# Optimization experiments

Measured on AMD Instinct MI355X. Metric: run time of the kernel, lower is better.

## Reference

```python
import jax, jax.numpy as jnp
import numpy as np

N, B, E, H, G, L = 128, 2, 512, 1024, 50, 3
RBF_RADIUS = 12.0
AVG_LEN = 60.0


def _resmlp(h, Win, bin_, Wh, bh, Wout, bout):
    # input proj + activation, residual hidden blocks, linear head
    h = jax.nn.gelu(h @ Win + bin_, approximate=False)
    for i in range(Wh.shape[0]):  # fixed small number of layers
        h = h + jax.nn.gelu(h @ Wh[i] + bh[i], approximate=False)
    return h @ Wout + bout


def setup_inputs() -> dict:
    key = jax.random.key(0)
    ks = jax.random.split(key, 20)
    s_in = 1.0 / np.sqrt(3 * E)
    s_h = 1.0 / np.sqrt(H)
    s_g = 1.0 / np.sqrt(G)
    return {
        'x': jax.random.normal(ks[0], (N, B, E), jnp.float32),
        'dist': jax.random.uniform(ks[1], (N, N, B), jnp.float32),
        'vec_hat': jax.random.normal(ks[2], (N, N, B, 3), jnp.float32),
        'mask': jnp.ones((B, N), dtype=bool),
        'rbf_W': jax.random.normal(ks[3], (G, E), jnp.float32) * s_g,
        'rbf_b': jnp.zeros((E,), jnp.float32),
        'e_Win': jax.random.normal(ks[4], (3 * E, H), jnp.float32) * s_in,
        'e_bin': jnp.zeros((H,), jnp.float32),
        'e_Wh': jax.random.normal(ks[5], (L, H, H), jnp.float32) * s_h,
        'e_bh': jnp.zeros((L, H), jnp.float32),
        'e_Wout': jax.random.normal(ks[6], (H, 1), jnp.float32) * s_h,
        'e_bout': jnp.zeros((1,), jnp.float32),
        'f_Win': jax.random.normal(ks[7], (3 * E, H), jnp.float32) * s_in,
        'f_bin': jnp.zeros((H,), jnp.float32),
        'f_Wh': jax.random.normal(ks[8], (L, H, H), jnp.float32) * s_h,
        'f_bh': jnp.zeros((L, H), jnp.float32),
        'f_Wout': jax.random.normal(ks[9], (H, 1), jnp.float32) * s_h,
        'f_bout': jnp.zeros((1,), jnp.float32),
    }


def reference(x, dist, vec_hat, mask, rbf_W, rbf_b, e_Win, e_bin, e_Wh, e_bh,
              e_Wout, e_bout, f_Win, f_bin, f_Wh, f_bh, f_Wout, f_bout):
    # Gaussian RBF expansion + linear projection to embed_dim
    offset = jnp.linspace(0.0, RBF_RADIUS, G)
    coeff = -0.5 / (offset[1] - offset[0]) ** 2
    g = jnp.exp(coeff * (dist[..., None] - offset) ** 2)       # (N,N,B,G)
    rbf = g @ rbf_W + rbf_b                                    # (N,N,B,E)

    # all-pairs concat feature: [x_i, x_j, rbf_ij]  -> (N,N,B,3E)
    feat = jnp.concatenate([
        jnp.broadcast_to(x[:, None], rbf.shape),
        jnp.broadcast_to(x[None, :], rbf.shape),
        rbf,
    ], axis=-1)

    entries = (mask.T[:, None] & mask.T[None, :])[..., None].astype(feat.dtype)  # (N,N,B,1)

    energy_pairs = _resmlp(feat, e_Win, e_bin, e_Wh, e_bh, e_Wout, e_bout)       # (N,N,B,1)
    force_pairs = _resmlp(feat, f_Win, f_bin, f_Wh, f_bh, f_Wout, f_bout) * vec_hat  # (N,N,B,3)

    energy = (energy_pairs * entries).sum((0, 1)) / AVG_LEN ** 2  # (B,1)
    forces = (force_pairs * entries).sum(0) / AVG_LEN             # (N,B,3)
    # torch: forces.transpose(0,1)[mask]; mask is all-True here, so this is a reshape
    forces = jnp.swapaxes(forces, 0, 1).reshape(-1, 3)            # (B*N,3)
    return energy, forces
```

## Files before the change

kernel.cpp:

```cpp
#include <hip/hip_runtime.h>
#include <stdint.h>

typedef __bf16 bf16x8 __attribute__((ext_vector_type(8)));
typedef __bf16 bf16x4 __attribute__((ext_vector_type(4)));
typedef float  f32x4  __attribute__((ext_vector_type(4)));
typedef unsigned int u32;

__device__ __forceinline__ void gl_lds16(const void* gptr, void* lptr) {
    __builtin_amdgcn_global_load_lds(
        (const __attribute__((address_space(1))) u32*)gptr,
        (__attribute__((address_space(3))) u32*)lptr,
        16, 0, 0);
}

__device__ __forceinline__ float gelu_f(float x) {
    float u = 0.7978845608f * x * (1.0f + 0.044715f * x * x);
    float e = __expf(2.0f * u);
    float t = 1.0f - 2.0f / (e + 1.0f);
    return 0.5f * x * (1.0f + t);
}

#define MEMFENCE __asm__ __volatile__("" ::: "memory")

__global__ void zero_out(float* __restrict__ o, int n) {
    int i = blockIdx.x * 256 + threadIdx.x;
    if (i < n) o[i] = 0.0f;
}

__global__ __launch_bounds__(256)
void transpose_multi(const float* __restrict__ src0, const float* __restrict__ src1,
                     __bf16* __restrict__ dst0, __bf16* __restrict__ dst1,
                     int K, int Ncols, int perBranch) {
    const int z = blockIdx.z;
    const int branch = z / perBranch;
    const int l = z - branch * perBranch;
    const size_t elems = (size_t)K * Ncols;
    const float* src = (branch ? src1 : src0) + (size_t)l * elems;
    __bf16* dst = (branch ? dst1 : dst0) + (size_t)l * elems;

    __shared__ float tile[64][65];
    const int bk = blockIdx.x * 64;
    const int bn = blockIdx.y * 64;
    const int tid = threadIdx.x;
    const int tr = tid >> 4;
    const int tc = (tid & 15) * 4;
#pragma unroll
    for (int p = 0; p < 4; ++p) {
        const int r = tr + p * 16;
        float4 v = *(const float4*)&src[(size_t)(bk + r) * Ncols + bn + tc];
        tile[r][tc] = v.x; tile[r][tc + 1] = v.y;
        tile[r][tc + 2] = v.z; tile[r][tc + 3] = v.w;
    }
    __syncthreads();
#pragma unroll
    for (int p = 0; p < 4; ++p) {
        const int rn = tr + p * 16;
        bf16x4 o;
        o[0] = (__bf16)tile[tc + 0][rn];
        o[1] = (__bf16)tile[tc + 1][rn];
        o[2] = (__bf16)tile[tc + 2][rn];
        o[3] = (__bf16)tile[tc + 3][rn];
        *(bf16x4*)&dst[(size_t)(bn + rn) * K + bk + tc] = o;
    }
}

__global__ void f32_to_bf16(const float* __restrict__ s, __bf16* __restrict__ d, int n) {
    int idx = blockIdx.x * 256 + threadIdx.x;
    if (idx * 4 < n) {
        float4 v = *(const float4*)(s + idx * 4);
        bf16x4 o;
        o[0] = (__bf16)v.x; o[1] = (__bf16)v.y; o[2] = (__bf16)v.z; o[3] = (__bf16)v.w;
        *(bf16x4*)(d + idx * 4) = o;
    }
}

__global__ void build_M1(const float* __restrict__ rbfW, const float* __restrict__ rbf_b,
                         __bf16* __restrict__ M1) {
    int t = blockIdx.x * 256 + threadIdx.x;
    int r = t >> 8;
    int c = (t & 255) * 2;
    float v0 = 0.f, v1 = 0.f;
    if (r < 50)       { v0 = rbfW[r * 512 + c]; v1 = rbfW[r * 512 + c + 1]; }
    else if (r == 50) { v0 = rbf_b[c];          v1 = rbf_b[c + 1]; }
    M1[r * 512 + c] = (__bf16)v0;
    M1[r * 512 + c + 1] = (__bf16)v1;
}

__global__ __launch_bounds__(256)
void build_G(const float* __restrict__ dist, __bf16* __restrict__ G) {
    const int t = threadIdx.x;
    const int row = blockIdx.x * 32 + (t >> 3);
    const int c0 = (t & 7) * 8;
    const float sp = 12.0f / 49.0f;
    const float coeff = -0.5f / (sp * sp);
    const float d = dist[row];
    bf16x8 v;
#pragma unroll
    for (int q = 0; q < 8; ++q) {
        const int k = c0 + q;
        float val;
        if (k < 50)       { float tt = d - (float)k * sp; val = __expf(coeff * tt * tt); }
        else if (k == 50) val = 1.0f;
        else              val = 0.0f;
        v[q] = (__bf16)val;
    }
    *(bf16x8*)(G + (size_t)row * 64 + c0) = v;
}

template <int NK, int NBN, int MODE, bool DUAL, int MINW, bool SWZ>
__global__ __launch_bounds__(256, MINW)
void gemm_k(const __bf16* __restrict__ A0, const __bf16* __restrict__ A1,
            const __bf16* __restrict__ B0, const __bf16* __restrict__ B1,
            int lda, int ldb, int ldc,
            const float* __restrict__ bias0, const float* __restrict__ bias1,
            __bf16* __restrict__ C0, __bf16* __restrict__ C1,
            float* __restrict__ Cf0, float* __restrict__ Cf1,
            const float* __restrict__ P0, const float* __restrict__ P1,
            const float* __restrict__ wout0, const float* __restrict__ wout1,
            float* __restrict__ dot0, float* __restrict__ dot1) {
    constexpr int NBS = (NBN == 16) ? 4 : (NBN == 8) ? 3 : 0;
    __shared__ __align__(16) __bf16 As[3][128 * 32];
    __shared__ __align__(16) __bf16 Bs[3][128 * 32];

    const int tid = threadIdx.x;
    int bn, bm, branch = 0;
    if constexpr (SWZ) {
        const int x = blockIdx.x & 7;
        const int slot = blockIdx.x >> 3;
        bn = slot & (NBN - 1);
        int grp = x + ((slot >> NBS) << 3);
        if constexpr (DUAL) {
            const int half = (gridDim.x >> NBS) >> 1;
            branch = (grp >= half);
            if (branch) grp -= half;
        }
        bm = grp;
    } else {
        int f2 = blockIdx.x;
        if constexpr (DUAL) {
            const int half = gridDim.x >> 1;
            branch = (f2 >= half);
            if (branch) f2 -= half;
        }
        bn = f2 & (NBN - 1);
        bm = f2 >> NBS;
    }
    const int w = tid >> 6;
    const int lane = tid & 63;

    const __bf16* Ab = (DUAL && branch) ? A1 : A0;
    const __bf16* Bb = (DUAL && branch) ? B1 : B0;

    const int r0 = tid >> 2;
    const int s0 = tid & 3;
    const char* gA0 = (const char*)Ab + (size_t)(bm * 128 + r0) * lda + s0 * 16;
    const char* gA1 = gA0 + (size_t)64 * lda;
    const char* gB0 = (const char*)Bb + (size_t)(bn * 128 + r0) * ldb + s0 * 16;
    const char* gB1 = gB0 + (size_t)64 * ldb;

    char* lA0 = (char*)&As[0][0] + w * 1024;
    char* lA1 = (char*)&As[1][0] + w * 1024;
    char* lA2 = (char*)&As[2][0] + w * 1024;
    char* lB0 = (char*)&Bs[0][0] + w * 1024;
    char* lB1 = (char*)&Bs[1][0] + w * 1024;
    char* lB2 = (char*)&Bs[2][0] + w * 1024;

    const int wm = (w >> 1) & 1;
    const int wn = w & 1;
    const int lm = lane & 15;
    const int ko = (lane >> 4) << 3;
    const int fo = (wm * 64 + lm) * 32 + ko;
    const int go = (wn * 64 + lm) * 32 + ko;
    const __bf16* pA0 = &As[0][0] + fo;
    const __bf16* pA1 = &As[1][0] + fo;
    const __bf16* pA2 = &As[2][0] + fo;
    const __bf16* pB0 = &Bs[0][0] + go;
    const __bf16* pB1 = &Bs[1][0] + go;
    const __bf16* pB2 = &Bs[2][0] + go;

    f32x4 acc[4][4];
    const f32x4 zero = {0.0f, 0.0f, 0.0f, 0.0f};
#pragma unroll
    for (int i = 0; i < 4; ++i)
#pragma unroll
        for (int j = 0; j < 4; ++j) acc[i][j] = zero;

    auto stage = [&](int buf) {
        char* la = (buf == 0) ? lA0 : (buf == 1) ? lA1 : lA2;
        char* lb = (buf == 0) ? lB0 : (buf == 1) ? lB1 : lB2;
        gl_lds16(gA0, la); gl_lds16(gA1, la + 4096);
        gl_lds16(gB0, lb); gl_lds16(gB1, lb + 4096);
        gA0 += 64; gA1 += 64; gB0 += 64; gB1 += 64;
    };
    auto compute = [&](int buf) {
        const __bf16* pa = (buf == 0) ? pA0 : (buf == 1) ? pA1 : pA2;
        const __bf16* pb = (buf == 0) ? pB0 : (buf == 1) ? pB1 : pB2;
        bf16x8 af[4], bfg[4];
#pragma unroll
        for (int i = 0; i < 4; ++i) {
            af[i]  = *(const bf16x8*)(pa + i * 512);
            bfg[i] = *(const bf16x8*)(pb + i * 512);
        }
#pragma unroll
        for (int mi = 0; mi < 4; ++mi)
#pragma unroll
            for (int ni = 0; ni < 4; ++ni)
                acc[mi][ni] = __builtin_amdgcn_mfma_f32_16x16x32_bf16(
                    af[mi], bfg[ni], acc[mi][ni], 0, 0, 0);
    };
    auto iterstep = [&](int cbuf, int sbuf) {
        MEMFENCE;
        __builtin_amdgcn_s_waitcnt(0xF74);
        __builtin_amdgcn_s_barrier();
        MEMFENCE;
        compute(cbuf);
        MEMFENCE;
        stage(sbuf);
        MEMFENCE;
    };

    stage(0);
    stage(1);
    constexpr int NIT = NK - 2;
    constexpr int NG = NIT / 3;
    constexpr int NR = NIT % 3;
    for (int g = 0; g < NG; ++g) {
        iterstep(0, 2);
        iterstep(1, 0);
        iterstep(2, 1);
    }
    if constexpr (NR >= 1) iterstep(0, 2);
    if constexpr (NR >= 2) iterstep(1, 0);
    MEMFENCE;
    __builtin_amdgcn_s_waitcnt(0xF74);
    __builtin_amdgcn_s_barrier();
    MEMFENCE;
    compute((NK - 2) % 3);
    MEMFENCE;
    __builtin_amdgcn_s_waitcnt(0xF70);
    __builtin_amdgcn_s_barrier();
    MEMFENCE;
    compute((NK - 1) % 3);

    const int col0 = bn * 128 + wn * 64 + lm;
    const int row0 = bm * 128 + wm * 64 + ((lane >> 4) << 2);
    const int ldaE = lda >> 1;

    float rowdot[16];
    if constexpr (MODE == 1) {
#pragma unroll
        for (int q = 0; q < 16; ++q) rowdot[q] = 0.0f;
    }

    const bool side = (MODE == 2) && (bn >= 8);
    const float* bp = (MODE == 2) ? (side ? bias1 : bias0)
                                  : ((DUAL && branch) ? bias1 : bias0);
    __bf16* Cout = (MODE == 2) ? (side ? C1 : C0)
                               : ((DUAL && branch) ? C1 : C0);
    const float* woutb = (MODE == 1) ? ((DUAL && branch) ? wout1 : wout0) : nullptr;

#pragma unroll
    for (int ni = 0; ni < 4; ++ni) {
        const int gn = col0 + ni * 16;
        const int gnl = (MODE == 2) ? (gn & 1023) : gn;
        float bv = 0.0f;
        if constexpr (MODE <= 2) bv = bp[gnl];
        float wv = 0.0f;
        if constexpr (MODE == 1) wv = woutb[gn];

        float res[16];
        if constexpr (MODE == 0 || MODE == 1) {
#pragma unroll
            for (int mi = 0; mi < 4; ++mi)
#pragma unroll
                for (int rr = 0; rr < 4; ++rr)
                    res[mi * 4 + rr] =
                        (float)Ab[(size_t)(row0 + mi * 16 + rr) * ldaE + gn];
        } else if constexpr (MODE == 2) {
#pragma unroll
            for (int mi = 0; mi < 4; ++mi)
#pragma unroll
                for (int rr = 0; rr < 4; ++rr) {
                    const int gm = row0 + mi * 16 + rr;
                    const int p0row = ((gm >> 8) << 1) | (gm & 1);
                    const int p1row = gm & 255;
                    res[mi * 4 + rr] = P0[(size_t)p0row * 2048 + gn]
                                     + P1[(size_t)p1row * 2048 + gn];
                }
        }
        MEMFENCE;

#pragma unroll
        for (int mi = 0; mi < 4; ++mi) {
#pragma unroll
            for (int rr = 0; rr < 4; ++rr) {
                const int gm = row0 + mi * 16 + rr;
                const float a = acc[mi][ni][rr];
                if constexpr (MODE == 0) {
                    float v = gelu_f(a + bv) + res[mi * 4 + rr];
                    Cout[(size_t)gm * ldc + gn] = (__bf16)v;
                } else if constexpr (MODE == 1) {
                    float v = gelu_f(a + bv) + res[mi * 4 + rr];
                    rowdot[mi * 4 + rr] += v * wv;
                } else if constexpr (MODE == 2) {
                    float v = a + bv + res[mi * 4 + rr];
                    Cout[(size_t)gm * ldc + gnl] = (__bf16)gelu_f(v);
                } else if constexpr (MODE == 3) {
                    float* Cfw = (DUAL && branch) ? Cf1 : Cf0;
                    Cfw[(size_t)gm * ldc + gn] = a;
                } else {
                    C0[(size_t)gm * ldc + gn] = (__bf16)a;
                }
            }
        }
    }

    if constexpr (MODE == 1) {
#pragma unroll
        for (int s = 1; s < 16; s <<= 1)
#pragma unroll
            for (int q = 0; q < 16; ++q) rowdot[q] += __shfl_xor(rowdot[q], s);
        if (lm == 0) {
            float* dotb = (DUAL && branch) ? dot1 : dot0;
            float* dp = dotb + (size_t)(bn * 2 + wn) * 32768 + row0;
#pragma unroll
            for (int q = 0; q < 16; ++q)
                dp[(q >> 2) * 16 + (q & 3)] = rowdot[q];
        }
    }
}

template <int MODE, bool DUAL>
__global__ __launch_bounds__(512, 2)
void gemm256(const __bf16* __restrict__ A0, const __bf16* __restrict__ A1,
             const __bf16* __restrict__ B0, const __bf16* __restrict__ B1,
             const float* __restrict__ bias0, const float* __restrict__ bias1,
             __bf16* __restrict__ C0, __bf16* __restrict__ C1,
             const float* __restrict__ wout0, const float* __restrict__ wout1,
             float* __restrict__ dot0, float* __restrict__ dot1) {
    __shared__ __align__(16) char ldsbuf[131072];

    const int tid = threadIdx.x;
    const int nxg = gridDim.x >> 3;
    const int id = (blockIdx.x & 7) * nxg + (blockIdx.x >> 3);
    const int bn = id & 3;
    int rest = id >> 2;
    int branch = 0;
    if constexpr (DUAL) { branch = rest >> 7; rest &= 127; }
    const int bm = rest;

    const __bf16* __restrict__ Ab = (DUAL && branch) ? A1 : A0;
    const __bf16* __restrict__ Bb = (DUAL && branch) ? B1 : B0;

    const int w = tid >> 6;
    const int lane = tid & 63;

    const int srow = tid >> 3;
    const int scol = ((tid & 7) * 16) ^ (((tid >> 3) & 7) << 4);
    const char* gA = (const char*)Ab + (size_t)(bm * 256 + srow) * 2048 + scol;
    const char* gB = (const char*)Bb + (size_t)(bn * 256 + srow) * 2048 + scol;
    char* stBase = ldsbuf + w * 1024;

    auto stageTile = [&](int kt, int buf) {
        const size_t ko = (size_t)kt * 128;
        char* d = stBase + buf * 65536;
        gl_lds16(gA + ko,              d);
        gl_lds16(gA + ko +  64 * 2048, d + 8192);
        gl_lds16(gA + ko + 128 * 2048, d + 16384);
        gl_lds16(gA + ko + 192 * 2048, d + 24576);
        gl_lds16(gB + ko,              d + 32768);
        gl_lds16(gB + ko +  64 * 2048, d + 40960);
        gl_lds16(gB + ko + 128 * 2048, d + 49152);
        gl_lds16(gB + ko + 192 * 2048, d + 57344);
    };

    const int wm = w >> 2, wn = w & 3;
    const int lm = lane & 15, lq = lane >> 4;
    const int xorm = (lm & 7) << 4;
    const int rA0 = (wm * 128 + lm) * 128;
    const int rB0 = 32768 + (wn * 64 + lm) * 128;
    const int offk0 = (lq * 16) ^ xorm;
    const int offk1 = (64 + lq * 16) ^ xorm;

    f32x4 acc[8][4];
    const f32x4 zero = {0.0f, 0.0f, 0.0f, 0.0f};
#pragma unroll
    for (int i = 0; i < 8; ++i)
#pragma unroll
        for (int j = 0; j < 4; ++j) acc[i][j] = zero;

    auto body = [&](int kt, bool last) {
        const char* Lb = ldsbuf + (kt & 1) * 65536;
        MEMFENCE;
        if (last) __builtin_amdgcn_s_waitcnt(0xF70);
        else      __builtin_amdgcn_s_waitcnt(0xF78);
        __builtin_amdgcn_s_barrier();
        MEMFENCE;
        bf16x8 a0[8], b0[4], a1[8], b1[4];
#pragma unroll
        for (int mi = 0; mi < 8; ++mi)
            a0[mi] = *(const bf16x8*)(Lb + rA0 + mi * 2048 + offk0);
#pragma unroll
        for (int ni = 0; ni < 4; ++ni)
            b0[ni] = *(const bf16x8*)(Lb + rB0 + ni * 2048 + offk0);
        __builtin_amdgcn_s_setprio(1);
#pragma unroll
        for (int mi = 0; mi < 4; ++mi)
#pragma unroll
            for (int ni = 0; ni < 4; ++ni)
                acc[mi][ni] = __builtin_amdgcn_mfma_f32_16x16x32_bf16(
                    a0[mi], b0[ni], acc[mi][ni], 0, 0, 0);
        __builtin_amdgcn_s_setprio(0);
#pragma unroll
        for (int mi = 0; mi < 8; ++mi)
            a1[mi] = *(const bf16x8*)(Lb + rA0 + mi * 2048 + offk1);
#pragma unroll
        for (int ni = 0; ni < 4; ++ni)
            b1[ni] = *(const bf16x8*)(Lb + rB0 + ni * 2048 + offk1);
        __builtin_amdgcn_s_setprio(1);
#pragma unroll
        for (int mi = 4; mi < 8; ++mi)
#pragma unroll
            for (int ni = 0; ni < 4; ++ni)
                acc[mi][ni] = __builtin_amdgcn_mfma_f32_16x16x32_bf16(
                    a0[mi], b0[ni], acc[mi][ni], 0, 0, 0);
        __builtin_amdgcn_s_setprio(0);
        MEMFENCE;
        __builtin_amdgcn_s_waitcnt(0xC07F);
        __builtin_amdgcn_s_barrier();
        MEMFENCE;
        if (!last && kt < 14) stageTile(kt + 2, kt & 1);
        MEMFENCE;
        __builtin_amdgcn_s_setprio(1);
#pragma unroll
        for (int mi = 0; mi < 4; ++mi)
#pragma unroll
            for (int ni = 0; ni < 4; ++ni)
                acc[mi][ni] = __builtin_amdgcn_mfma_f32_16x16x32_bf16(
                    a1[mi], b1[ni], acc[mi][ni], 0, 0, 0);
#pragma unroll
        for (int mi = 4; mi < 8; ++mi)
#pragma unroll
            for (int ni = 0; ni < 4; ++ni)
                acc[mi][ni] = __builtin_amdgcn_mfma_f32_16x16x32_bf16(
                    a1[mi], b1[ni], acc[mi][ni], 0, 0, 0);
        __builtin_amdgcn_s_setprio(0);
    };

    stageTile(0, 0);
    stageTile(1, 1);
    for (int kt = 0; kt < 15; ++kt) body(kt, false);
    body(15, true);

    const int row0 = bm * 256 + wm * 128 + lq * 4;
    const int col0 = bn * 256 + wn * 64 + lm;
    const float* __restrict__ bp = (DUAL && branch) ? bias1 : bias0;
    float bv[4];
#pragma unroll
    for (int ni = 0; ni < 4; ++ni) bv[ni] = bp[col0 + ni * 16];

    if constexpr (MODE == 0) {
        __bf16* __restrict__ Cw = (DUAL && branch) ? C1 : C0;
#pragma unroll
        for (int mi = 0; mi < 8; ++mi) {
            float res[16];
#pragma unroll
            for (int ni = 0; ni < 4; ++ni)
#pragma unroll
                for (int rr = 0; rr < 4; ++rr)
                    res[ni * 4 + rr] =
                        (float)Ab[(size_t)(row0 + mi * 16 + rr) * 1024 + col0 + ni * 16];
            MEMFENCE;
#pragma unroll
            for (int ni = 0; ni < 4; ++ni)
#pragma unroll
                for (int rr = 0; rr < 4; ++rr) {
                    float v = gelu_f(acc[mi][ni][rr] + bv[ni]) + res[ni * 4 + rr];
                    Cw[(size_t)(row0 + mi * 16 + rr) * 1024 + col0 + ni * 16] = (__bf16)v;
                }
        }
    } else {
        const float* __restrict__ wb = (DUAL && branch) ? wout1 : wout0;
        float wv[4];
#pragma unroll
        for (int ni = 0; ni < 4; ++ni) wv[ni] = wb[col0 + ni * 16];
        float rowdot[32];
#pragma unroll
        for (int q = 0; q < 32; ++q) rowdot[q] = 0.0f;
#pragma unroll
        for (int mi = 0; mi < 8; ++mi) {
            float res[16];
#pragma unroll
            for (int ni = 0; ni < 4; ++ni)
#pragma unroll
                for (int rr = 0; rr < 4; ++rr)
                    res[ni * 4 + rr] =
                        (float)Ab[(size_t)(row0 + mi * 16 + rr) * 1024 + col0 + ni * 16];
            MEMFENCE;
#pragma unroll
            for (int ni = 0; ni < 4; ++ni)
#pragma unroll
                for (int rr = 0; rr < 4; ++rr) {
                    float v = gelu_f(acc[mi][ni][rr] + bv[ni]) + res[ni * 4 + rr];
                    rowdot[mi * 4 + rr] += v * wv[ni];
                }
        }
#pragma unroll
        for (int s = 1; s < 16; s <<= 1)
#pragma unroll
            for (int q = 0; q < 32; ++q) rowdot[q] += __shfl_xor(rowdot[q], s);
        if (lm == 0) {
            float* __restrict__ db = (DUAL && branch) ? dot1 : dot0;
            float* dp = db + (size_t)(bn * 4 + wn) * 32768 + bm * 256 + wm * 128;
#pragma unroll
            for (int mi = 0; mi < 8; ++mi)
#pragma unroll
                for (int rr = 0; rr < 4; ++rr)
                    dp[mi * 16 + lq * 4 + rr] = rowdot[mi * 4 + rr];
        }
    }
}

__global__ __launch_bounds__(128)
void finalize(const float* __restrict__ dot_e, const float* __restrict__ dot_f,
              const float* __restrict__ eb, const float* __restrict__ fb,
              const float* __restrict__ vec, float* __restrict__ out) {
    const int bj = blockIdx.x;
    const int bb = bj >> 7, jj = bj & 127;
    const int i = threadIdx.x;
    const int m = (i * 128 + jj) * 2 + bb;
    float e = eb[0], f = fb[0];
#pragma unroll
    for (int s = 0; s < 16; ++s) {
        e += dot_e[(size_t)s * 32768 + m];
        f += dot_f[(size_t)s * 32768 + m];
    }
    f *= (1.0f / 60.0f);
    float fx = f * vec[(size_t)m * 3 + 0];
    float fy = f * vec[(size_t)m * 3 + 1];
    float fz = f * vec[(size_t)m * 3 + 2];
#pragma unroll
    for (int off = 32; off > 0; off >>= 1) {
        e  += __shfl_down(e, off);
        fx += __shfl_down(fx, off);
        fy += __shfl_down(fy, off);
        fz += __shfl_down(fz, off);
    }
    __shared__ float red[2][4];
    const int wv = i >> 6, lane = i & 63;
    if (lane == 0) { red[wv][0] = e; red[wv][1] = fx; red[wv][2] = fy; red[wv][3] = fz; }
    __syncthreads();
    if (i == 0) {
        atomicAdd(&out[bb], (red[0][0] + red[1][0]) * (1.0f / 3600.0f));
        float* fo = out + 2 + bj * 3;
        fo[0] = red[0][1] + red[1][1];
        fo[1] = red[0][2] + red[1][2];
        fo[2] = red[0][3] + red[1][3];
    }
}

extern "C" void kernel_launch(void* const* d_in, const int* in_sizes, int n_in,
                              void* d_out, int out_size, void* d_ws, size_t ws_size,
                              hipStream_t stream) {
    const float* x     = (const float*)d_in[0];
    const float* dist  = (const float*)d_in[1];
    const float* vec   = (const float*)d_in[2];
    const float* rbfW  = (const float*)d_in[4];
    const float* rbf_b = (const float*)d_in[5];
    const float* eWin  = (const float*)d_in[6];
    const float* ebin  = (const float*)d_in[7];
    const float* eWh   = (const float*)d_in[8];
    const float* ebh   = (const float*)d_in[9];
    const float* eWout = (const float*)d_in[10];
    const float* ebout = (const float*)d_in[11];
    const float* fWin  = (const float*)d_in[12];
    const float* fbin  = (const float*)d_in[13];
    const float* fWh   = (const float*)d_in[14];
    const float* fbh   = (const float*)d_in[15];
    const float* fWout = (const float*)d_in[16];
    const float* fbout = (const float*)d_in[17];
    float* out = (float*)d_out;

    char* p = (char*)d_ws;
    __bf16* WinTcat = (__bf16*)p;
    __bf16* eWinT = WinTcat;          p += (size_t)1024 * 1536 * 2;
    __bf16* fWinT = (__bf16*)p;       p += (size_t)1024 * 1536 * 2;
    __bf16* eWhT0 = (__bf16*)p;       p += (size_t)3 * 1024 * 1024 * 2;
    __bf16* fWhT0 = (__bf16*)p;       p += (size_t)3 * 1024 * 1024 * 2;
    __bf16* xb  = (__bf16*)p;         p += (size_t)256 * 512 * 2;
    __bf16* M1  = (__bf16*)p;         p += (size_t)128 * 512 * 2;
    __bf16* WgT = (__bf16*)p;         p += (size_t)2048 * 128 * 2;
    __bf16* G   = (__bf16*)p;         p += (size_t)32768 * 64 * 2;
    float* P0   = (float*)p;          p += (size_t)256 * 2048 * 4;
    float* P1   = (float*)p;          p += (size_t)256 * 2048 * 4;
    float* dot_e = (float*)p;         p += (size_t)16 * 32768 * 4;
    float* dot_f = (float*)p;         p += (size_t)16 * 32768 * 4;
    const size_t SLAB = (size_t)32768 * 1024 * 2;
    __bf16* he0 = (__bf16*)p;         p += SLAB;
    __bf16* hf0 = (__bf16*)p;         p += SLAB;
    __bf16* hAe = (__bf16*)p;         p += SLAB;
    __bf16* hAf = hAe;
    const bool dualHidden = ((size_t)(p - (char*)d_ws) + SLAB) <= ws_size;
    if (dualHidden) hAf = (__bf16*)p;

    zero_out<<<dim3(4), dim3(256), 0, stream>>>(out, 770);

    transpose_multi<<<dim3(24, 16, 2), dim3(256), 0, stream>>>(
        eWin, fWin, eWinT, fWinT, 1536, 1024, 1);
    transpose_multi<<<dim3(16, 16, 6), dim3(256), 0, stream>>>(
        eWh, fWh, eWhT0, fWhT0, 1024, 1024, 3);
    f32_to_bf16<<<dim3(128), dim3(256), 0, stream>>>(x, xb, 131072);
    build_M1<<<dim3(128), dim3(256), 0, stream>>>(rbfW, rbf_b, M1);
    build_G<<<dim3(1024), dim3(256), 0, stream>>>(dist, G);

    const dim3 blk(256);
    gemm_k<16, 16, 3, true, 3, false><<<dim3(64), blk, 0, stream>>>(
        xb, xb, WinTcat, WinTcat + 512, 1024, 3072, 2048,
        nullptr, nullptr, nullptr, nullptr, P0, P1,
        nullptr, nullptr, nullptr, nullptr, nullptr, nullptr);
    gemm_k<16, 1, 4, false, 3, false><<<dim3(16), blk, 0, stream>>>(
        WinTcat + 1024, nullptr, M1, nullptr, 3072, 1024, 128,
        nullptr, nullptr, WgT, nullptr, nullptr, nullptr,
        nullptr, nullptr, nullptr, nullptr, nullptr, nullptr);
    gemm_k<2, 16, 2, false, 3, true><<<dim3(4096), blk, 0, stream>>>(
        G, nullptr, WgT, nullptr, 128, 256, 1024,
        ebin, fbin, he0, hf0, nullptr, nullptr, P0, P1,
        nullptr, nullptr, nullptr, nullptr);

    const dim3 blk512(512);
    if (dualHidden) {
        gemm256<0, true><<<dim3(1024), blk512, 0, stream>>>(
            he0, hf0, eWhT0, fWhT0, ebh + 0, fbh + 0,
            hAe, hAf, nullptr, nullptr, nullptr, nullptr);
        gemm256<0, true><<<dim3(1024), blk512, 0, stream>>>(
            hAe, hAf, eWhT0 + (size_t)1048576, fWhT0 + (size_t)1048576,
            ebh + 1024, fbh + 1024, he0, hf0, nullptr, nullptr, nullptr, nullptr);
        gemm256<1, true><<<dim3(1024), blk512, 0, stream>>>(
            he0, hf0, eWhT0 + (size_t)2 * 1048576, fWhT0 + (size_t)2 * 1048576,
            ebh + 2048, fbh + 2048, nullptr, nullptr,
            eWout, fWout, dot_e, dot_f);
    } else {
        gemm256<0, false><<<dim3(512), blk512, 0, stream>>>(
            he0, nullptr, eWhT0, nullptr, ebh + 0, nullptr,
            hAe, nullptr, nullptr, nullptr, nullptr, nullptr);
        gemm256<0, false><<<dim3(512), blk512, 0, stream>>>(
            hAe, nullptr, eWhT0 + (size_t)1048576, nullptr, ebh + 1024, nullptr,
            he0, nullptr, nullptr, nullptr, nullptr, nullptr);
        gemm256<1, false><<<dim3(512), blk512, 0, stream>>>(
            he0, nullptr, eWhT0 + (size_t)2 * 1048576, nullptr, ebh + 2048, nullptr,
            nullptr, nullptr, eWout, nullptr, dot_e, nullptr);
        gemm256<0, false><<<dim3(512), blk512, 0, stream>>>(
            hf0, nullptr, fWhT0, nullptr, fbh + 0, nullptr,
            hAf, nullptr, nullptr, nullptr, nullptr, nullptr);
        gemm256<0, false><<<dim3(512), blk512, 0, stream>>>(
            hAf, nullptr, fWhT0 + (size_t)1048576, nullptr, fbh + 1024, nullptr,
            hf0, nullptr, nullptr, nullptr, nullptr, nullptr);
        gemm256<1, false><<<dim3(512), blk512, 0, stream>>>(
            hf0, nullptr, fWhT0 + (size_t)2 * 1048576, nullptr, fbh + 2048, nullptr,
            nullptr, nullptr, fWout, nullptr, dot_f, nullptr);
    }

    finalize<<<dim3(256), dim3(128), 0, stream>>>(dot_e, dot_f, ebout, fbout, vec, out);
}
```

Baseline: 716.1 us.

## Switch GEMM mainloop to a four-stage LDS ring with half-depth K tiles

The 256x256 GEMM mainloop moves from two 64-element-deep K tiles in LDS to four 32-element-deep K tiles. Loads are issued three tiles ahead, and each iteration now needs one waitcnt+barrier instead of two. The LDS swizzle and the per-thread staging addressing are rewritten for the 64-byte row pitch. The aim is to keep more global loads in flight and cut barrier stalls, at the cost of twice as many iterations and fewer MFMAs between barriers.

Result: slower. 748.4 us (+4.5%).

```diff
diff --git a/kernel.cpp b/kernel.cpp
--- a/kernel.cpp
+++ b/kernel.cpp
@@ -330,6 +330,9 @@
     }
 }
 
+#define WBAR(imm) do { MEMFENCE; __builtin_amdgcn_s_waitcnt(imm); \
+                       __builtin_amdgcn_s_barrier(); MEMFENCE; } while (0)
+
 template <int MODE, bool DUAL>
 __global__ __launch_bounds__(512, 2)
 void gemm256(const __bf16* __restrict__ A0, const __bf16* __restrict__ A1,
@@ -355,32 +358,25 @@
     const int w = tid >> 6;
     const int lane = tid & 63;
 
-    const int srow = tid >> 3;
-    const int scol = ((tid & 7) * 16) ^ (((tid >> 3) & 7) << 4);
+    const int srow = tid >> 2;
+    const int scol = ((tid & 3) << 4) ^ (((tid >> 3) & 3) << 4);
     const char* gA = (const char*)Ab + (size_t)(bm * 256 + srow) * 2048 + scol;
     const char* gB = (const char*)Bb + (size_t)(bn * 256 + srow) * 2048 + scol;
-    char* stBase = ldsbuf + w * 1024;
-
-    auto stageTile = [&](int kt, int buf) {
-        const size_t ko = (size_t)kt * 128;
-        char* d = stBase + buf * 65536;
-        gl_lds16(gA + ko,              d);
-        gl_lds16(gA + ko +  64 * 2048, d + 8192);
-        gl_lds16(gA + ko + 128 * 2048, d + 16384);
-        gl_lds16(gA + ko + 192 * 2048, d + 24576);
-        gl_lds16(gB + ko,              d + 32768);
-        gl_lds16(gB + ko +  64 * 2048, d + 40960);
-        gl_lds16(gB + ko + 128 * 2048, d + 49152);
-        gl_lds16(gB + ko + 192 * 2048, d + 57344);
+
+    auto stageT = [&](int kt, int buf) {
+        const size_t ko = (size_t)kt * 64;
+        char* d = ldsbuf + buf * 32768 + w * 1024;
+        gl_lds16(gA + ko,          d);
+        gl_lds16(gA + ko + 262144, d + 8192);
+        gl_lds16(gB + ko,          d + 16384);
+        gl_lds16(gB + ko + 262144, d + 24576);
     };
 
     const int wm = w >> 2, wn = w & 3;
     const int lm = lane & 15, lq = lane >> 4;
-    const int xorm = (lm & 7) << 4;
-    const int rA0 = (wm * 128 + lm) * 128;
-    const int rB0 = 32768 + (wn * 64 + lm) * 128;
-    const int offk0 = (lq * 16) ^ xorm;
-    const int offk1 = (64 + lq * 16) ^ xorm;
+    const int swz = ((lm >> 1) & 3) << 4;
+    const int rA = (wm * 128 + lm) * 64 + ((lq * 16) ^ swz);
+    const int rB = 16384 + (wn * 64 + lm) * 64 + ((lq * 16) ^ swz);
 
     f32x4 acc[8][4];
     const f32x4 zero = {0.0f, 0.0f, 0.0f, 0.0f};
@@ -389,68 +385,49 @@
 #pragma unroll
         for (int j = 0; j < 4; ++j) acc[i][j] = zero;
 
-    auto body = [&](int kt, bool last) {
-        const char* Lb = ldsbuf + (kt & 1) * 65536;
+    auto body = [&](int kt, int cbuf, int sbuf, bool dostage) {
+        const char* Lb = ldsbuf + cbuf * 32768;
+        if (dostage) stageT(kt + 3, sbuf);
         MEMFENCE;
-        if (last) __builtin_amdgcn_s_waitcnt(0xF70);
-        else      __builtin_amdgcn_s_waitcnt(0xF78);
-        __builtin_amdgcn_s_barrier();
-        MEMFENCE;
-        bf16x8 a0[8], b0[4], a1[8], b1[4];
+        bf16x8 a[8], b[4];
+#pragma unroll
+        for (int ni = 0; ni < 4; ++ni)
+            b[ni] = *(const bf16x8*)(Lb + rB + ni * 1024);
 #pragma unroll
         for (int mi = 0; mi < 8; ++mi)
-            a0[mi] = *(const bf16x8*)(Lb + rA0 + mi * 2048 + offk0);
-#pragma unroll
-        for (int ni = 0; ni < 4; ++ni)
-            b0[ni] = *(const bf16x8*)(Lb + rB0 + ni * 2048 + offk0);
+            a[mi] = *(const bf16x8*)(Lb + rA + mi * 1024);
         __builtin_amdgcn_s_setprio(1);
 #pragma unroll
         for (int mi = 0; mi < 4; ++mi)
 #pragma unroll
             for (int ni = 0; ni < 4; ++ni)
                 acc[mi][ni] = __builtin_amdgcn_mfma_f32_16x16x32_bf16(
-                    a0[mi], b0[ni], acc[mi][ni], 0, 0, 0);
+                    a[mi], b[ni], acc[mi][ni], 0, 0, 0);
         __builtin_amdgcn_s_setprio(0);
-#pragma unroll
-        for (int mi = 0; mi < 8; ++mi)
-            a1[mi] = *(const bf16x8*)(Lb + rA0 + mi * 2048 + offk1);
-#pragma unroll
-        for (int ni = 0; ni < 4; ++ni)
-            b1[ni] = *(const bf16x8*)(Lb + rB0 + ni * 2048 + offk1);
         __builtin_amdgcn_s_setprio(1);
 #pragma unroll
         for (int mi = 4; mi < 8; ++mi)
 #pragma unroll
             for (int ni = 0; ni < 4; ++ni)
                 acc[mi][ni] = __builtin_amdgcn_mfma_f32_16x16x32_bf16(
-                    a0[mi], b0[ni], acc[mi][ni], 0, 0, 0);
-        __builtin_amdgcn_s_setprio(0);
-        MEMFENCE;
-        __builtin_amdgcn_s_waitcnt(0xC07F);
-        __builtin_amdgcn_s_barrier();
-        MEMFENCE;
-        if (!last && kt < 14) stageTile(kt + 2, kt & 1);
-        MEMFENCE;
-        __builtin_amdgcn_s_setprio(1);
-#pragma unroll
-        for (int mi = 0; mi < 4; ++mi)
-#pragma unroll
-            for (int ni = 0; ni < 4; ++ni)
-                acc[mi][ni] = __builtin_amdgcn_mfma_f32_16x16x32_bf16(
-                    a1[mi], b1[ni], acc[mi][ni], 0, 0, 0);
-#pragma unroll
-        for (int mi = 4; mi < 8; ++mi)
-#pragma unroll
-            for (int ni = 0; ni < 4; ++ni)
-                acc[mi][ni] = __builtin_amdgcn_mfma_f32_16x16x32_bf16(
-                    a1[mi], b1[ni], acc[mi][ni], 0, 0, 0);
+                    a[mi], b[ni], acc[mi][ni], 0, 0, 0);
         __builtin_amdgcn_s_setprio(0);
     };
 
-    stageTile(0, 0);
-    stageTile(1, 1);
-    for (int kt = 0; kt < 15; ++kt) body(kt, false);
-    body(15, true);
+    stageT(0, 0);
+    stageT(1, 1);
+    stageT(2, 2);
+    for (int g = 0; g < 7; ++g) {
+        const int k0 = g * 4;
+        WBAR(0xF78); body(k0 + 0, 0, 3, true);
+        WBAR(0xF78); body(k0 + 1, 1, 0, true);
+        WBAR(0xF78); body(k0 + 2, 2, 1, true);
+        WBAR(0xF78); body(k0 + 3, 3, 2, true);
+    }
+    WBAR(0xF78); body(28, 0, 3, true);
+    WBAR(0xF78); body(29, 1, 0, false);
+    WBAR(0xF74); body(30, 2, 1, false);
+    WBAR(0xF70); body(31, 3, 2, false);
 
     const int row0 = bm * 256 + wm * 128 + lq * 4;
     const int col0 = bn * 256 + wn * 64 + lm;
```
